# Kernel optimization log

Hardware: AMD Instinct MI355X
Metric: run time of the kernel (lower is better)

## Reference

```python
import jax, jax.numpy as jnp
import numpy as np

D = 1024   # d_model
H = 16     # n_heads
S = 2048   # seq_len
HD = D // H  # head_dim = 64
B = 1


def setup_inputs() -> dict:
    key = jax.random.key(0)
    ks = jax.random.split(key, 10)
    s = 0.02
    return {
        "x": jax.random.normal(ks[0], (B, S * D), dtype=jnp.float32),
        "Wq": jax.random.normal(ks[1], (D, D), dtype=jnp.float32) * s,
        "bq": jnp.zeros((D,), dtype=jnp.float32),
        "Wk": jax.random.normal(ks[2], (D, D), dtype=jnp.float32) * s,
        "bk": jnp.zeros((D,), dtype=jnp.float32),
        "Wv": jax.random.normal(ks[3], (D, D), dtype=jnp.float32) * s,
        "bv": jnp.zeros((D,), dtype=jnp.float32),
        "Wo": jax.random.normal(ks[4], (D, D), dtype=jnp.float32) * s,
        "bo": jnp.zeros((D,), dtype=jnp.float32),
        "rel_table": jax.random.normal(ks[5], (2 * S - 1, HD), dtype=jnp.float32),
    }


def reference(x, Wq, bq, Wk, bk, Wv, bv, Wo, bo, rel_table):
    b = x.shape[0]
    x3 = x.reshape(b, S, D)
    # projections; split into heads -> [b, H, S, HD]
    def heads(t):
        return t.reshape(b, S, H, HD).transpose(0, 2, 1, 3)
    Q = heads(x3 @ Wq + bq)
    K = heads(x3 @ Wk + bk)
    V = heads(x3 @ Wv + bv)

    scores = jnp.einsum('bhid,bhjd->bhij', Q, K) / np.sqrt(HD).astype(np.float32)

    # relative position index: clamp(i - j + S - 1, 0, 2S-2)
    pos = jnp.arange(S)
    idx = jnp.clip(pos[:, None] - pos[None, :] + S - 1, 0, 2 * S - 2)  # [S, S]
    # contract Q with the raw table once, then gather per (i, j)
    # (same math as einsum('bhid,ijd->bhij', Q, table[idx]) but avoids [S,S,HD])
    qrel = jnp.einsum('bhid,rd->bhir', Q, rel_table)          # [b, H, S, 2S-1]
    rel_scores = jnp.take_along_axis(qrel, idx[None, None, :, :], axis=-1)  # [b,H,S,S]

    attn = jax.nn.softmax(scores + rel_scores, axis=-1)
    # dropout is identity in eval mode
    out = jnp.einsum('bhij,bhjd->bhid', attn, V)              # [b, H, S, HD]
    out = out.transpose(0, 2, 1, 3).reshape(b, S, D)
    return (out @ Wo + bo).reshape(b, -1)
```

## Files before the change

### kernel.cpp

```cpp
#include <hip/hip_runtime.h>
#include <hip/hip_bf16.h>

#define SEQ 2048
#define DM  1024
#define NH  16
#define HDM 64

typedef __hip_bfloat16 bf16;
typedef __bf16 bhalf8 __attribute__((ext_vector_type(8)));
typedef float floatx4 __attribute__((ext_vector_type(4)));

__device__ __forceinline__ void async_cp16(const void* g, void* l) {
  __builtin_amdgcn_global_load_lds(
      (const __attribute__((address_space(1))) void*)g,
      (__attribute__((address_space(3))) void*)l, 16, 0, 0);
}

__global__ __launch_bounds__(256) void prep(
    const float* __restrict__ x, const float* __restrict__ T,
    const float* __restrict__ W0, const float* __restrict__ W1,
    const float* __restrict__ W2, const float* __restrict__ W3,
    bf16* __restrict__ xbf, bf16* __restrict__ Tbf, bf16* __restrict__ WtBase)
{
  __shared__ float tile[64][69];
  const int b = blockIdx.x;
  const int tid = threadIdx.x;
  if (b < 2048) {
    int c = b * 256 + tid;
    float4 v = *(const float4*)&x[(size_t)c * 4];
    union { bf16 h[4]; float2 f; } u;
    u.h[0] = __float2bfloat16(v.x); u.h[1] = __float2bfloat16(v.y);
    u.h[2] = __float2bfloat16(v.z); u.h[3] = __float2bfloat16(v.w);
    *(float2*)&xbf[(size_t)c * 4] = u.f;
  } else if (b < 2304) {
    int ct = (b - 2048) * 256 + tid;
    union { bf16 h[4]; float2 f; } u;
#pragma unroll
    for (int e = 0; e < 4; ++e) {
      int se = ct * 4 + e;
      if (se >= 4095 * 64) se -= 64;
      u.h[e] = __float2bfloat16(T[se]);
    }
    *(float2*)&Tbf[(size_t)ct * 4] = u.f;
  } else {
    int tb = b - 2304;
    int z = tb >> 8, rem = tb & 255;
    const float* W = (z == 0) ? W0 : (z == 1) ? W1 : (z == 2) ? W2 : W3;
    bf16* Wt = WtBase + (size_t)z * DM * DM;
    const int kb = (rem >> 4) * 64, nb = (rem & 15) * 64;
    const int r = tid >> 4, c4 = (tid & 15) * 4;
#pragma unroll
    for (int rr = 0; rr < 4; ++rr) {
      float4 v = *(const float4*)&W[(size_t)(kb + rr * 16 + r) * DM + nb + c4];
      tile[rr * 16 + r][c4 + 0] = v.x; tile[rr * 16 + r][c4 + 1] = v.y;
      tile[rr * 16 + r][c4 + 2] = v.z; tile[rr * 16 + r][c4 + 3] = v.w;
    }
    __syncthreads();
    const int w = tid >> 6, l = tid & 63;
#pragma unroll
    for (int i = 0; i < 16; ++i) {
      int n = nb + w * 16 + i;
      Wt[(size_t)n * DM + kb + l] = __float2bfloat16(tile[l][w * 16 + i]);
    }
  }
}

__device__ __forceinline__ void gemm64_core(
    const bf16* __restrict__ A, const bf16* __restrict__ Bt,
    bf16* As, bf16* Bs, int bm, int bn, floatx4 (&acc)[4])
{
  const int tid = threadIdx.x;
  const int lane = tid & 63;
  const int w = tid >> 6;
  const int ln15 = lane & 15, quad = lane >> 4;
  const int qs8  = (quad ^ ((ln15 >> 1) & 3)) * 8;
  const int srow = tid >> 2;
  const int scol = ((tid & 3) ^ ((tid >> 3) & 3)) * 8;

  for (int k0 = 0; k0 < DM; k0 += 64) {
    async_cp16(A  + (size_t)(bm + srow) * DM + k0 + scol,      As + tid * 8);
    async_cp16(A  + (size_t)(bm + srow) * DM + k0 + 32 + scol, As + 2048 + tid * 8);
    async_cp16(Bt + (size_t)(bn + srow) * DM + k0 + scol,      Bs + tid * 8);
    async_cp16(Bt + (size_t)(bn + srow) * DM + k0 + 32 + scol, Bs + 2048 + tid * 8);
    __syncthreads();
#pragma unroll
    for (int kk = 0; kk < 2; ++kk) {
      bhalf8 af = *(bhalf8*)&As[kk * 2048 + (w * 16 + ln15) * 32 + qs8];
      bhalf8 bfr[4];
#pragma unroll
      for (int j = 0; j < 4; ++j)
        bfr[j] = *(bhalf8*)&Bs[kk * 2048 + (j * 16 + ln15) * 32 + qs8];
#pragma unroll
      for (int j = 0; j < 4; ++j)
        acc[j] = __builtin_amdgcn_mfma_f32_16x16x32_bf16(af, bfr[j], acc[j], 0, 0, 0);
    }
    __syncthreads();
  }
}

__global__ __launch_bounds__(256) void gemm_qkv128(
    const bf16* __restrict__ A, const bf16* __restrict__ Wt3,
    const float* __restrict__ bq, const float* __restrict__ bk,
    const float* __restrict__ bv, bf16* __restrict__ outbase)
{
  __shared__ __align__(16) bf16 As[128 * 64];
  __shared__ __align__(16) bf16 Bs[128 * 64];
  const int z = blockIdx.z;
  const bf16* Bt = Wt3 + (size_t)z * DM * DM;
  const float* bias = (z == 0) ? bq : (z == 1) ? bk : bv;
  const float kscale = (z == 1) ? 0.125f : 1.0f;
  bf16* C = outbase + (size_t)z * SEQ * DM;
  const int bm = blockIdx.y * 128, bn = blockIdx.x * 128;
  const int tid = threadIdx.x;
  const int lane = tid & 63, w = tid >> 6;
  const int ln15 = lane & 15, quad = lane >> 4;
  const int wr = (w >> 1) * 64, wc = (w & 1) * 64;

  floatx4 acc[4][4];
#pragma unroll
  for (int mi = 0; mi < 4; ++mi)
#pragma unroll
    for (int nj = 0; nj < 4; ++nj) acc[mi][nj] = (floatx4){0.f, 0.f, 0.f, 0.f};

  for (int k0 = 0; k0 < DM; k0 += 64) {
#pragma unroll
    for (int t = 0; t < 4; ++t) {
      int cid = t * 256 + tid;
      int row = cid >> 3;
      int scol = ((cid & 7) ^ (row & 7)) * 8;
      async_cp16(A  + (size_t)(bm + row) * DM + k0 + scol, As + cid * 8);
      async_cp16(Bt + (size_t)(bn + row) * DM + k0 + scol, Bs + cid * 8);
    }
    __syncthreads();
#pragma unroll
    for (int kk = 0; kk < 2; ++kk) {
      const int chs = ((kk * 4 + quad) ^ (ln15 & 7)) * 8;
      bhalf8 af[4], bfr[4];
#pragma unroll
      for (int mi = 0; mi < 4; ++mi)
        af[mi] = *(bhalf8*)&As[(wr + mi * 16 + ln15) * 64 + chs];
#pragma unroll
      for (int nj = 0; nj < 4; ++nj)
        bfr[nj] = *(bhalf8*)&Bs[(wc + nj * 16 + ln15) * 64 + chs];
#pragma unroll
      for (int mi = 0; mi < 4; ++mi)
#pragma unroll
        for (int nj = 0; nj < 4; ++nj)
          acc[mi][nj] = __builtin_amdgcn_mfma_f32_16x16x32_bf16(
              af[mi], bfr[nj], acc[mi][nj], 0, 0, 0);
    }
    __syncthreads();
  }

#pragma unroll
  for (int nj = 0; nj < 4; ++nj) {
    int col = bn + wc + nj * 16 + ln15;
    float bv_ = bias[col];
#pragma unroll
    for (int mi = 0; mi < 4; ++mi) {
#pragma unroll
      for (int r = 0; r < 4; ++r) {
        int row = bm + wr + mi * 16 + quad * 4 + r;
        float v = (acc[mi][nj][r] + bv_) * kscale;
        if (z < 2)
          C[((size_t)(col >> 6) * SEQ + row) * HDM + (col & 63)] = __float2bfloat16(v);
        else
          C[(size_t)col * SEQ + row] = __float2bfloat16(v);
      }
    }
  }
}

__global__ __launch_bounds__(256) void gemm_out(
    const bf16* __restrict__ A, const bf16* __restrict__ Bt,
    const float* __restrict__ bias, float* __restrict__ C)
{
  __shared__ __align__(16) bf16 As[64 * 64];
  __shared__ __align__(16) bf16 Bs[64 * 64];
  const int bm = blockIdx.y * 64, bn = blockIdx.x * 64;
  floatx4 acc[4];
#pragma unroll
  for (int j = 0; j < 4; ++j) acc[j] = (floatx4){0.f, 0.f, 0.f, 0.f};
  gemm64_core(A, Bt, As, Bs, bm, bn, acc);

  const int lane = threadIdx.x & 63;
  const int w = threadIdx.x >> 6;
  const int ln15 = lane & 15, quad = lane >> 4;
#pragma unroll
  for (int j = 0; j < 4; ++j) {
    int col = bn + j * 16 + ln15;
    float bv_ = bias[col];
#pragma unroll
    for (int r = 0; r < 4; ++r) {
      int row = bm + w * 16 + quad * 4 + r;
      C[(size_t)row * DM + col] = acc[j][r] + bv_;
    }
  }
}

__global__ __launch_bounds__(256, 2) void attn_flash(
    const bf16* __restrict__ Q, const bf16* __restrict__ K,
    const bf16* __restrict__ Vt, const bf16* __restrict__ Tb,
    bf16* __restrict__ Opart, float* __restrict__ lws)
{
  const int i0   = blockIdx.x * 64;
  const int h    = blockIdx.y;
  const int z    = blockIdx.z;
  const int tid  = threadIdx.x;
  const int lane = tid & 63;
  const int wrow = (tid >> 6) * 16;
  const int ln15 = lane & 15;
  const int quad = lane >> 4;

  __shared__ __align__(16) unsigned char smem[75264];
  bf16*  Ps  = (bf16*)(smem + 49152);
  float* S2c = (float*)(smem + 58368);
  bf16*  Qs  = (bf16*)(smem + 58368);

  const bf16* Qg = Q  + ((size_t)h * SEQ + i0) * HDM;
  const bf16* Kg = K  + (size_t)h * SEQ * HDM;
  const bf16* Vg = Vt + (size_t)h * HDM * SEQ;

  const int r4 = tid >> 2, c8 = (tid & 3) * 8;
  auto stage = [&](int jt_, int b) {
    int j0_ = jt_ * 64;
    int rb_ = i0 - j0_ + SEQ - HDM;
    bf16* Kd = (bf16*)smem + b * 4096;
    bf16* Vd = (bf16*)smem + 8192 + b * 4096;
    bf16* Td = (bf16*)smem + 16384 + b * 4096;
    async_cp16(Kg + (size_t)(j0_ + r4) * HDM + c8,        Kd + tid * 8);
    async_cp16(Kg + (size_t)(j0_ + r4) * HDM + 32 + c8,   Kd + 2048 + tid * 8);
    async_cp16(Vg + (size_t)r4 * SEQ + j0_ + c8,          Vd + tid * 8);
    async_cp16(Vg + (size_t)r4 * SEQ + j0_ + 32 + c8,     Vd + 2048 + tid * 8);
    async_cp16(Tb + (size_t)(rb_ + r4) * HDM + c8,        Td + tid * 8);
    async_cp16(Tb + (size_t)(rb_ + r4) * HDM + 32 + c8,   Td + 2048 + tid * 8);
  };

  const int jt0 = z * 16;
  stage(jt0, 0);

#pragma unroll
  for (int t = 0; t < 2; ++t) {
    int id = tid + t * 256;
    int r = id >> 3, c = (id & 7) * 8;
    *(float4*)&Qs[r * 72 + c] = *(const float4*)&Qg[(size_t)r * HDM + c];
  }
  __syncthreads();

  const bhalf8 aq0 = *(bhalf8*)&Qs[(wrow + ln15) * 72 + quad * 8];
  const bhalf8 aq1 = *(bhalf8*)&Qs[(wrow + ln15) * 72 + quad * 8 + 32];

  floatx4 o[4];
  float lsum[4];
#pragma unroll
  for (int c = 0; c < 4; ++c) { o[c] = (floatx4){0.f, 0.f, 0.f, 0.f}; lsum[c] = 0.f; }

  const int rb0 = i0 - jt0 * 64 + SEQ - HDM;
  floatx4 carry[4];
#pragma unroll
  for (int ct = 0; ct < 4; ++ct) {
    const bf16* tr = Tb + (size_t)(rb0 + 64 + ct * 16 + ln15) * HDM + quad * 8;
    bhalf8 b0 = *(const bhalf8*)tr;
    bhalf8 b1 = *(const bhalf8*)(tr + 32);
    floatx4 a = (floatx4){0.f, 0.f, 0.f, 0.f};
    a = __builtin_amdgcn_mfma_f32_16x16x32_bf16(aq0, b0, a, 0, 0, 0);
    a = __builtin_amdgcn_mfma_f32_16x16x32_bf16(aq1, b1, a, 0, 0, 0);
    carry[ct] = a;
  }

  int cur = 0;
  for (int jt = jt0; jt < jt0 + 16; ++jt) {
    __syncthreads();
    if (jt + 1 < jt0 + 16) stage(jt + 1, cur ^ 1);
    const bf16* Ksc = (bf16*)smem + cur * 4096;
    const bf16* Vsc = (bf16*)smem + 8192 + cur * 4096;
    const bf16* Tsc = (bf16*)smem + 16384 + cur * 4096;

    floatx4 fresh[4];
#pragma unroll
    for (int ct = 0; ct < 4; ++ct) {
      bhalf8 b0 = *(bhalf8*)&Tsc[(ct * 16 + ln15) * 32 + quad * 8];
      bhalf8 b1 = *(bhalf8*)&Tsc[2048 + (ct * 16 + ln15) * 32 + quad * 8];
      floatx4 a = (floatx4){0.f, 0.f, 0.f, 0.f};
      a = __builtin_amdgcn_mfma_f32_16x16x32_bf16(aq0, b0, a, 0, 0, 0);
      a = __builtin_amdgcn_mfma_f32_16x16x32_bf16(aq1, b1, a, 0, 0, 0);
      fresh[ct] = a;
    }
#pragma unroll
    for (int ct = 0; ct < 4; ++ct) {
      int t = ct * 16 + ln15;
#pragma unroll
      for (int r = 0; r < 4; ++r) {
        int row = wrow + quad * 4 + r;
        if (t >= row) S2c[row * 66 + (row + 63 - t)] = fresh[ct][r];
        else          S2c[row * 66 + (row - 1 - t)] = carry[ct][r];
      }
      carry[ct] = fresh[ct];
    }

#pragma unroll
    for (int ct = 0; ct < 4; ++ct) {
      floatx4 s2f;
#pragma unroll
      for (int r = 0; r < 4; ++r)
        s2f[r] = S2c[(wrow + quad * 4 + r) * 66 + ct * 16 + ln15];
      bhalf8 b0 = *(bhalf8*)&Ksc[(ct * 16 + ln15) * 32 + quad * 8];
      bhalf8 b1 = *(bhalf8*)&Ksc[2048 + (ct * 16 + ln15) * 32 + quad * 8];
      floatx4 a = __builtin_amdgcn_mfma_f32_16x16x32_bf16(aq0, b0, s2f, 0, 0, 0);
      a = __builtin_amdgcn_mfma_f32_16x16x32_bf16(aq1, b1, a, 0, 0, 0);
#pragma unroll
      for (int r = 0; r < 4; ++r) {
        float p = __expf(a[r]);
        lsum[r] += p;
        Ps[(wrow + quad * 4 + r) * 72 + ct * 16 + ln15] = __float2bfloat16(p);
      }
    }

    bhalf8 ap0 = *(bhalf8*)&Ps[(wrow + ln15) * 72 + quad * 8];
    bhalf8 ap1 = *(bhalf8*)&Ps[(wrow + ln15) * 72 + quad * 8 + 32];
#pragma unroll
    for (int ct = 0; ct < 4; ++ct) {
      bhalf8 b0 = *(bhalf8*)&Vsc[(ct * 16 + ln15) * 32 + quad * 8];
      bhalf8 b1 = *(bhalf8*)&Vsc[2048 + (ct * 16 + ln15) * 32 + quad * 8];
      o[ct] = __builtin_amdgcn_mfma_f32_16x16x32_bf16(ap0, b0, o[ct], 0, 0, 0);
      o[ct] = __builtin_amdgcn_mfma_f32_16x16x32_bf16(ap1, b1, o[ct], 0, 0, 0);
    }
    cur ^= 1;
  }

  bf16* Oz = Opart + (size_t)z * SEQ * DM;
#pragma unroll
  for (int r = 0; r < 4; ++r) {
    float l = lsum[r];
    l += __shfl_xor(l, 1); l += __shfl_xor(l, 2);
    l += __shfl_xor(l, 4); l += __shfl_xor(l, 8);
    float inv = 1.f / l;
    int row = i0 + wrow + quad * 4 + r;
#pragma unroll
    for (int ct = 0; ct < 4; ++ct)
      Oz[(size_t)row * DM + h * HDM + ct * 16 + ln15] =
          __float2bfloat16(o[ct][r] * inv);
    if (ln15 == 0)
      lws[((size_t)z * NH + h) * SEQ + row] = l;
  }
}

__global__ __launch_bounds__(256) void attn_merge(
    const bf16* __restrict__ O0, const bf16* __restrict__ O1,
    const float* __restrict__ lws, bf16* __restrict__ O)
{
  const int i = blockIdx.x;
  const int tid = threadIdx.x;
  __shared__ float w0s[NH], w1s[NH];
  if (tid < NH) {
    float l0 = lws[((size_t)0 * NH + tid) * SEQ + i];
    float l1 = lws[((size_t)1 * NH + tid) * SEQ + i];
    float inv = 1.f / (l0 + l1);
    w0s[tid] = l0 * inv; w1s[tid] = l1 * inv;
  }
  __syncthreads();
  const int d = tid * 4;
  const float w0 = w0s[d >> 6], w1 = w1s[d >> 6];
  union { bf16 h[4]; float2 f; } a0, a1, ov;
  a0.f = *(const float2*)&O0[(size_t)i * DM + d];
  a1.f = *(const float2*)&O1[(size_t)i * DM + d];
#pragma unroll
  for (int e = 0; e < 4; ++e)
    ov.h[e] = __float2bfloat16(w0 * __bfloat162float(a0.h[e]) +
                               w1 * __bfloat162float(a1.h[e]));
  *(float2*)&O[(size_t)i * DM + d] = ov.f;
}

extern "C" void kernel_launch(void* const* d_in, const int* in_sizes, int n_in,
                              void* d_out, int out_size, void* d_ws, size_t ws_size,
                              hipStream_t stream) {
  const float* x   = (const float*)d_in[0];
  const float* Wq  = (const float*)d_in[1];
  const float* bq  = (const float*)d_in[2];
  const float* Wk  = (const float*)d_in[3];
  const float* bk  = (const float*)d_in[4];
  const float* Wv  = (const float*)d_in[5];
  const float* bv  = (const float*)d_in[6];
  const float* Wo  = (const float*)d_in[7];
  const float* bo  = (const float*)d_in[8];
  const float* rel = (const float*)d_in[9];
  float* out = (float*)d_out;

  const size_t SD = (size_t)SEQ * DM;
  bf16* qws = (bf16*)d_ws;
  bf16* kws = qws + SD;
  bf16* vws = kws + SD;
  bf16* ows = vws + SD;
  bf16* xbf = ows + SD;
  bf16* wt  = xbf + SD;
  bf16* tbf = wt + 4 * (size_t)DM * DM;
  bf16* opart = tbf + (size_t)4096 * HDM;
  float* lws  = (float*)(opart + 2 * SD);

  prep<<<3328, 256, 0, stream>>>(x, rel, Wq, Wk, Wv, Wo, xbf, tbf, wt);
  gemm_qkv128<<<dim3(8, 16, 3), 256, 0, stream>>>(xbf, wt, bq, bk, bv, qws);
  attn_flash<<<dim3(SEQ / 64, NH, 2), 256, 0, stream>>>(qws, kws, vws, tbf,
                                                        opart, lws);
  attn_merge<<<SEQ, 256, 0, stream>>>(opart, opart + SD, lws, ows);
  gemm_out<<<dim3(16, 32), 256, 0, stream>>>(ows, wt + 3 * (size_t)DM * DM, bo, out);
}
```

Measured before the change: 203.1 us.

## Fuse split-KV merge into output projection GEMM and swizzle P tile in LDS

Removes the separate attn_merge kernel and performs the weighted combination of the two partial attention outputs while loading the A tile of the output-projection GEMM. This saves a kernel launch and a full write-then-read round trip of the merged bf16 activations. The cost is that each of the 16 column blocks now redoes the merge work and reads both partial buffers through synchronous loads instead of async copies. Separately, attn_flash writes and reads the P tile through a rotated column layout to reduce LDS bank conflicts.

```diff
diff --git a/kernel.cpp b/kernel.cpp
--- a/kernel.cpp
+++ b/kernel.cpp
@@ -65,39 +65,6 @@
   }
 }
 
-__device__ __forceinline__ void gemm64_core(
-    const bf16* __restrict__ A, const bf16* __restrict__ Bt,
-    bf16* As, bf16* Bs, int bm, int bn, floatx4 (&acc)[4])
-{
-  const int tid = threadIdx.x;
-  const int lane = tid & 63;
-  const int w = tid >> 6;
-  const int ln15 = lane & 15, quad = lane >> 4;
-  const int qs8  = (quad ^ ((ln15 >> 1) & 3)) * 8;
-  const int srow = tid >> 2;
-  const int scol = ((tid & 3) ^ ((tid >> 3) & 3)) * 8;
-
-  for (int k0 = 0; k0 < DM; k0 += 64) {
-    async_cp16(A  + (size_t)(bm + srow) * DM + k0 + scol,      As + tid * 8);
-    async_cp16(A  + (size_t)(bm + srow) * DM + k0 + 32 + scol, As + 2048 + tid * 8);
-    async_cp16(Bt + (size_t)(bn + srow) * DM + k0 + scol,      Bs + tid * 8);
-    async_cp16(Bt + (size_t)(bn + srow) * DM + k0 + 32 + scol, Bs + 2048 + tid * 8);
-    __syncthreads();
-#pragma unroll
-    for (int kk = 0; kk < 2; ++kk) {
-      bhalf8 af = *(bhalf8*)&As[kk * 2048 + (w * 16 + ln15) * 32 + qs8];
-      bhalf8 bfr[4];
-#pragma unroll
-      for (int j = 0; j < 4; ++j)
-        bfr[j] = *(bhalf8*)&Bs[kk * 2048 + (j * 16 + ln15) * 32 + qs8];
-#pragma unroll
-      for (int j = 0; j < 4; ++j)
-        acc[j] = __builtin_amdgcn_mfma_f32_16x16x32_bf16(af, bfr[j], acc[j], 0, 0, 0);
-    }
-    __syncthreads();
-  }
-}
-
 __global__ __launch_bounds__(256) void gemm_qkv128(
     const bf16* __restrict__ A, const bf16* __restrict__ Wt3,
     const float* __restrict__ bq, const float* __restrict__ bk,
@@ -171,21 +138,63 @@
   }
 }
 
-__global__ __launch_bounds__(256) void gemm_out(
-    const bf16* __restrict__ A, const bf16* __restrict__ Bt,
+__global__ __launch_bounds__(256) void gemm_out_fused(
+    const bf16* __restrict__ O0, const bf16* __restrict__ O1,
+    const float* __restrict__ lws, const bf16* __restrict__ Bt,
     const float* __restrict__ bias, float* __restrict__ C)
 {
   __shared__ __align__(16) bf16 As[64 * 64];
   __shared__ __align__(16) bf16 Bs[64 * 64];
   const int bm = blockIdx.y * 64, bn = blockIdx.x * 64;
+  const int tid = threadIdx.x;
+  const int lane = tid & 63;
+  const int w = tid >> 6;
+  const int ln15 = lane & 15, quad = lane >> 4;
+  const int qs8  = (quad ^ ((ln15 >> 1) & 3)) * 8;
+  const int srow = tid >> 2, sj = tid & 3;
+  const int swz  = (sj ^ ((srow >> 1) & 3)) * 8;
+  const int scol = (sj ^ ((tid >> 3) & 3)) * 8;
+  const int grow = bm + srow;
+
   floatx4 acc[4];
 #pragma unroll
   for (int j = 0; j < 4; ++j) acc[j] = (floatx4){0.f, 0.f, 0.f, 0.f};
-  gemm64_core(A, Bt, As, Bs, bm, bn, acc);
-
-  const int lane = threadIdx.x & 63;
-  const int w = threadIdx.x >> 6;
-  const int ln15 = lane & 15, quad = lane >> 4;
+
+  for (int k0 = 0; k0 < DM; k0 += 64) {
+    async_cp16(Bt + (size_t)(bn + srow) * DM + k0 + scol,      Bs + tid * 8);
+    async_cp16(Bt + (size_t)(bn + srow) * DM + k0 + 32 + scol, Bs + 2048 + tid * 8);
+    const int h = k0 >> 6;
+    float l0 = lws[(size_t)h * SEQ + grow];
+    float l1 = lws[(size_t)(NH + h) * SEQ + grow];
+    float inv = 1.f / (l0 + l1);
+    float w0 = l0 * inv, w1 = l1 * inv;
+#pragma unroll
+    for (int kk = 0; kk < 2; ++kk) {
+      const size_t off = (size_t)grow * DM + k0 + kk * 32 + sj * 8;
+      union { bf16 h8[8]; float4 f4; } a0, a1, m;
+      a0.f4 = *(const float4*)&O0[off];
+      a1.f4 = *(const float4*)&O1[off];
+#pragma unroll
+      for (int e = 0; e < 8; ++e)
+        m.h8[e] = __float2bfloat16(w0 * __bfloat162float(a0.h8[e]) +
+                                   w1 * __bfloat162float(a1.h8[e]));
+      *(float4*)&As[kk * 2048 + srow * 32 + swz] = m.f4;
+    }
+    __syncthreads();
+#pragma unroll
+    for (int kk = 0; kk < 2; ++kk) {
+      bhalf8 af = *(bhalf8*)&As[kk * 2048 + (w * 16 + ln15) * 32 + qs8];
+      bhalf8 bfr[4];
+#pragma unroll
+      for (int j = 0; j < 4; ++j)
+        bfr[j] = *(bhalf8*)&Bs[kk * 2048 + (j * 16 + ln15) * 32 + qs8];
+#pragma unroll
+      for (int j = 0; j < 4; ++j)
+        acc[j] = __builtin_amdgcn_mfma_f32_16x16x32_bf16(af, bfr[j], acc[j], 0, 0, 0);
+    }
+    __syncthreads();
+  }
+
 #pragma unroll
   for (int j = 0; j < 4; ++j) {
     int col = bn + j * 16 + ln15;
@@ -268,6 +277,11 @@
     carry[ct] = a;
   }
 
+  const int prow = wrow + ln15;
+  const int prot = ((prow >> 2) & 3) * 2;
+  const int pc0 = ((quad + prot) & 7) * 8;
+  const int pc1 = ((quad + 4 + prot) & 7) * 8;
+
   int cur = 0;
   for (int jt = jt0; jt < jt0 + 16; ++jt) {
     __syncthreads();
@@ -312,12 +326,14 @@
       for (int r = 0; r < 4; ++r) {
         float p = __expf(a[r]);
         lsum[r] += p;
-        Ps[(wrow + quad * 4 + r) * 72 + ct * 16 + ln15] = __float2bfloat16(p);
+        int row = wrow + quad * 4 + r;
+        int colp = ((ct * 16 + ln15) + ((row >> 2) & 3) * 16) & 63;
+        Ps[row * 72 + colp] = __float2bfloat16(p);
       }
     }
 
-    bhalf8 ap0 = *(bhalf8*)&Ps[(wrow + ln15) * 72 + quad * 8];
-    bhalf8 ap1 = *(bhalf8*)&Ps[(wrow + ln15) * 72 + quad * 8 + 32];
+    bhalf8 ap0 = *(bhalf8*)&Ps[prow * 72 + pc0];
+    bhalf8 ap1 = *(bhalf8*)&Ps[prow * 72 + pc1];
 #pragma unroll
     for (int ct = 0; ct < 4; ++ct) {
       bhalf8 b0 = *(bhalf8*)&Vsc[(ct * 16 + ln15) * 32 + quad * 8];
@@ -343,32 +359,6 @@
     if (ln15 == 0)
       lws[((size_t)z * NH + h) * SEQ + row] = l;
   }
-}
-
-__global__ __launch_bounds__(256) void attn_merge(
-    const bf16* __restrict__ O0, const bf16* __restrict__ O1,
-    const float* __restrict__ lws, bf16* __restrict__ O)
-{
-  const int i = blockIdx.x;
-  const int tid = threadIdx.x;
-  __shared__ float w0s[NH], w1s[NH];
-  if (tid < NH) {
-    float l0 = lws[((size_t)0 * NH + tid) * SEQ + i];
-    float l1 = lws[((size_t)1 * NH + tid) * SEQ + i];
-    float inv = 1.f / (l0 + l1);
-    w0s[tid] = l0 * inv; w1s[tid] = l1 * inv;
-  }
-  __syncthreads();
-  const int d = tid * 4;
-  const float w0 = w0s[d >> 6], w1 = w1s[d >> 6];
-  union { bf16 h[4]; float2 f; } a0, a1, ov;
-  a0.f = *(const float2*)&O0[(size_t)i * DM + d];
-  a1.f = *(const float2*)&O1[(size_t)i * DM + d];
-#pragma unroll
-  for (int e = 0; e < 4; ++e)
-    ov.h[e] = __float2bfloat16(w0 * __bfloat162float(a0.h[e]) +
-                               w1 * __bfloat162float(a1.h[e]));
-  *(float2*)&O[(size_t)i * DM + d] = ov.f;
 }
 
 extern "C" void kernel_launch(void* const* d_in, const int* in_sizes, int n_in,
@@ -401,6 +391,6 @@
   gemm_qkv128<<<dim3(8, 16, 3), 256, 0, stream>>>(xbf, wt, bq, bk, bv, qws);
   attn_flash<<<dim3(SEQ / 64, NH, 2), 256, 0, stream>>>(qws, kws, vws, tbf,
                                                         opart, lws);
-  attn_merge<<<SEQ, 256, 0, stream>>>(opart, opart + SD, lws, ows);
-  gemm_out<<<dim3(16, 32), 256, 0, stream>>>(ows, wt + 3 * (size_t)DM * DM, bo, out);
-}
+  gemm_out_fused<<<dim3(16, 32), 256, 0, stream>>>(
+      opart, opart + SD, lws, wt + 3 * (size_t)DM * DM, bo, out);
+}
```

Result: no change. 205.8 us (+1.3%).
